# Kernel optimization log

Measured on AMD Instinct MI355X. Metric: run time of the kernel, lower is better.

Reference implementation:

```python
import jax, jax.numpy as jnp
import numpy as np

B, G, D, H, L, MLP = 64, 512, 384, 6, 12, 4
DH = D // H
MASK_RATIO = 0.6
KEEP_RATIO = 0.1
PAD_VAL = -1.0
START_VAL = 1.0
POS_HID = 128
NEG = -1e9


def setup_inputs() -> dict:
    key = jax.random.key(0)
    ks = jax.random.split(key, 24)
    s = 0.02
    inp = {
        "x": jax.random.normal(ks[0], (B, G, D), jnp.float32),
        "center_points": jax.random.normal(ks[1], (B, G, 3), jnp.float32),
        "mask_noise": jax.random.uniform(ks[2], (B, G), jnp.float32),
        # pos embedder MLP: 3 -> 128 -> D
        "pos_w1": jax.random.normal(ks[3], (3, POS_HID), jnp.float32) * s,
        "pos_b1": jnp.zeros((POS_HID,), jnp.float32),
        "pos_w2": jax.random.normal(ks[4], (POS_HID, D), jnp.float32) * s,
        "pos_b2": jnp.zeros((D,), jnp.float32),
        # stacked per-layer transformer params
        "ln1_w": jnp.ones((L, D), jnp.float32),
        "ln1_b": jnp.zeros((L, D), jnp.float32),
        "qkv_w": jax.random.normal(ks[5], (L, D, 3 * D), jnp.float32) * s,
        "qkv_b": jnp.zeros((L, 3 * D), jnp.float32),
        "proj_w": jax.random.normal(ks[6], (L, D, D), jnp.float32) * s,
        "proj_b": jnp.zeros((L, D), jnp.float32),
        "ln2_w": jnp.ones((L, D), jnp.float32),
        "ln2_b": jnp.zeros((L, D), jnp.float32),
        "fc1_w": jax.random.normal(ks[7], (L, D, MLP * D), jnp.float32) * s,
        "fc1_b": jnp.zeros((L, MLP * D), jnp.float32),
        "fc2_w": jax.random.normal(ks[8], (L, MLP * D, D), jnp.float32) * s,
        "fc2_b": jnp.zeros((L, D), jnp.float32),
        # final LayerNorm
        "norm_w": jnp.ones((D,), jnp.float32),
        "norm_b": jnp.zeros((D,), jnp.float32),
    }
    return inp


def _layer_norm(h, w, b, eps=1e-5):
    mu = jnp.mean(h, axis=-1, keepdims=True)
    var = jnp.mean(jnp.square(h - mu), axis=-1, keepdims=True)
    return (h - mu) * jax.lax.rsqrt(var + eps) * w + b


def _random_mask(center, noise):
    # padding tokens: all coords equal PAD_VAL
    pad = jnp.all(center == PAD_VAL, axis=-1)                      # [B, G] bool
    if MASK_RATIO == 0:
        return jnp.zeros(pad.shape, bool), pad
    n = (G - jnp.sum(pad.astype(jnp.int32), axis=-1))              # non-padding count
    k = (n.astype(jnp.float32) * KEEP_RATIO).astype(jnp.int32)     # kept-first tokens
    m = ((n - k).astype(jnp.float32) * MASK_RATIO).astype(jnp.int32)
    M = jnp.max(m)
    j = jnp.arange(G)[None, :]
    # shuffle region [k, n): pick m random slots (uniform subset via rank of noise)
    region = (j >= k[:, None]) & (j < n[:, None])
    u = jnp.where(region, noise, jnp.inf)
    rank = jnp.argsort(jnp.argsort(u, axis=-1), axis=-1)
    shuf = (rank < m[:, None]) & region
    # tail of ones: positions [n, n + M - m)
    tail = (j >= n[:, None]) & (j < (n + M - m)[:, None])
    return shuf | tail, pad


def _attention(h, qw, qb, pw, pb, bias):
    qkv = (h @ qw + qb).reshape(B, G, 3, H, DH).transpose(2, 0, 3, 1, 4)
    q, k, v = qkv[0], qkv[1], qkv[2]                               # [B, H, G, DH]
    s = jnp.einsum('bhqd,bhkd->bhqk', q, k) * (DH ** -0.5) + bias
    a = jax.nn.softmax(s, axis=-1)
    o = jnp.einsum('bhqk,bhkd->bhqd', a, v).transpose(0, 2, 1, 3).reshape(B, G, D)
    return o @ pw + pb


def _forward(x, center_points, mask_noise,
             pos_w1, pos_b1, pos_w2, pos_b2,
             ln1_w, ln1_b, qkv_w, qkv_b, proj_w, proj_b,
             ln2_w, ln2_b, fc1_w, fc1_b, fc2_w, fc2_b,
             norm_w, norm_b):
    # shift right + start token
    start = jnp.full((B, 1, D), START_VAL, x.dtype)
    x = jnp.concatenate([start, x[:, :-1, :]], axis=1)
    # positional embedding of shifted centers + start-token pos
    pos = jax.nn.gelu(center_points[:, :-1, :] @ pos_w1 + pos_b1, approximate=False) @ pos_w2 + pos_b2
    pos = jnp.concatenate([jnp.full((B, 1, D), START_VAL, x.dtype), pos], axis=1)
    # causal | (random column mask & ~eye) attention mask
    triu = jnp.triu(jnp.ones((G, G), bool), 1)
    rand_mask, pad = _random_mask(center_points, mask_noise)
    eye = jnp.eye(G, dtype=bool)
    attn_mask = triu[None, :, :] | (rand_mask[:, None, :] & ~eye[None, :, :])   # [B, G, G]
    bias = jnp.where(attn_mask | pad[:, None, :], NEG, 0.0)[:, None, :, :]      # [B,1,G,G]

    def block(h, p):
        l1w, l1b, qw, qb, pw, pb, l2w, l2b, f1w, f1b, f2w, f2b = p
        h = h + pos
        h = h + _attention(_layer_norm(h, l1w, l1b), qw, qb, pw, pb, bias)
        h = h + (jax.nn.gelu(_layer_norm(h, l2w, l2b) @ f1w + f1b, approximate=False) @ f2w + f2b)
        return h, None

    x, _ = jax.lax.scan(block, x, (ln1_w, ln1_b, qkv_w, qkv_b, proj_w, proj_b,
                                   ln2_w, ln2_b, fc1_w, fc1_b, fc2_w, fc2_b))
    x = _layer_norm(x, norm_w, norm_b)
    return x, pad, attn_mask


def reference(x, center_points, mask_noise,
              pos_w1, pos_b1, pos_w2, pos_b2,
              ln1_w, ln1_b, qkv_w, qkv_b, proj_w, proj_b,
              ln2_w, ln2_b, fc1_w, fc1_b, fc2_w, fc2_b,
              norm_w, norm_b):
    out, pad, attn_mask = _forward(x, center_points, mask_noise,
                                   pos_w1, pos_b1, pos_w2, pos_b2,
                                   ln1_w, ln1_b, qkv_w, qkv_b, proj_w, proj_b,
                                   ln2_w, ln2_b, fc1_w, fc1_b, fc2_w, fc2_b,
                                   norm_w, norm_b)
    # torch repeat_interleave over heads -> [B*H, G, G]
    return out, pad, jnp.repeat(attn_mask, H, axis=0)
```

## Files before the change

### kernel.cpp

```cpp
#include <hip/hip_runtime.h>
#include <math.h>

typedef _Float16 f16;
typedef f16 f16x8 __attribute__((ext_vector_type(8)));
typedef float f32x4 __attribute__((ext_vector_type(4)));

#define NB 64
#define NG 512
#define ND 384
#define NH 6
#define NL 12
#define NDH 64
#define BG (NB * NG)
#define BGD (BG * ND)

#define OFF_WQKV   0
#define OFF_WPROJ  2654208
#define OFF_WFC1   3538944
#define OFF_WFC2   7077888
#define OFF_FLAGS  10616832
#define OFF_NKM    10625024
#define OFF_MMAX   10625216
#define OFF_POS    10625280
#define OFF_HID    23208192
#define OFF_Y      25305344
#define OFF_YBIG   31596800
#define OFF_QB     56762624
#define OFF_KB     63054080
#define OFF_VT     69345536
#define OFF_OB     75636992
#define OFF_W2T    81928448
#define OFF_HB     81953024

typedef __attribute__((address_space(3))) void lds_t;
typedef const __attribute__((address_space(1))) void gmem_t;
__device__ __forceinline__ void gload16(const void* g, void* l)
{
    __builtin_amdgcn_global_load_lds((gmem_t*)g, (lds_t*)l, 16, 0, 0);
}

__global__ __launch_bounds__(256)
void transpose_kernel(const float* __restrict__ src, f16* __restrict__ dst,
                      int K, int N)
{
    __shared__ float tile[32][33];
    const int l = blockIdx.z;
    const float* S = src + (size_t)l * K * N;
    f16* D = dst + (size_t)l * K * N;
    const int n0 = blockIdx.x * 32, k0 = blockIdx.y * 32;
    const int tx = threadIdx.x, ty = threadIdx.y;
#pragma unroll
    for (int i = 0; i < 32; i += 8)
        tile[ty + i][tx] = S[(size_t)(k0 + ty + i) * N + n0 + tx];
    __syncthreads();
#pragma unroll
    for (int i = 0; i < 32; i += 8)
        D[(size_t)(n0 + ty + i) * K + k0 + tx] = (f16)tile[tx][ty + i];
}

__global__ __launch_bounds__(256)
void dpos_a(const float* cen, const float* w1, const float* b1, f16* hid)
{
    const int idx = blockIdx.x * 256 + threadIdx.x;
    if (idx >= BG * 128) return;
    const int t = idx >> 7, k = idx & 127;
    const int g = t & (NG - 1);
    if (g == 0) { hid[idx] = (f16)0.f; return; }
    const float* c = cen + (size_t)(t - 1) * 3;
    const float hv = c[0] * w1[k] + c[1] * w1[128 + k] + c[2] * w1[256 + k] + b1[k];
    hid[idx] = (f16)(0.5f * hv * (1.0f + erff(hv * 0.70710678118654752f)));
}

__global__ __launch_bounds__(384)
void pos_fix(float* pos)
{
    const int b = blockIdx.x;
    pos[((size_t)b * NG) * ND + threadIdx.x] = 1.0f;
}

__global__ __launch_bounds__(512)
void dmask_a(const float* cen, float* pad_out, int* nkm)
{
    const int b = blockIdx.x, j = threadIdx.x;
    const float* c = cen + ((size_t)b * NG + j) * 3;
    const bool pad = (c[0] == -1.f) && (c[1] == -1.f) && (c[2] == -1.f);
    pad_out[b * NG + j] = pad ? 1.f : 0.f;
    if (j == 0) {
        int cnt = 0;
        for (int i = 0; i < NG; i++) {
            const float* ci = cen + ((size_t)b * NG + i) * 3;
            cnt += (ci[0] == -1.f && ci[1] == -1.f && ci[2] == -1.f) ? 1 : 0;
        }
        const int n = NG - cnt;
        const int k = (int)((float)n * 0.1f);
        const int m = (int)((float)(n - k) * 0.6f);
        nkm[b * 3] = n; nkm[b * 3 + 1] = k; nkm[b * 3 + 2] = m;
    }
}

__global__ void dmask_m(const int* nkm, int* Mmax)
{
    if (threadIdx.x == 0 && blockIdx.x == 0) {
        int M = 0;
        for (int b = 0; b < NB; b++) M = max(M, nkm[b * 3 + 2]);
        *Mmax = M;
    }
}

__global__ __launch_bounds__(512)
void dmask_b(const float* cen, const float* noi, const int* nkm,
             const int* Mmax, unsigned char* flags)
{
    const int b = blockIdx.x, j = threadIdx.x;
    const int n = nkm[b * 3], k = nkm[b * 3 + 1], m = nkm[b * 3 + 2];
    const int M = *Mmax;
    const float nz = noi[b * NG + j];
    const bool inreg = (j >= k) && (j < n);
    bool shuf = false;
    if (inreg) {
        int cnt = 0;
        for (int i = 0; i < NG; i++) {
            if (i < k || i >= n) continue;
            const float ui = noi[b * NG + i];
            cnt += (ui < nz) || (ui == nz && i < j);
        }
        shuf = cnt < m;
    }
    const float* c = cen + ((size_t)b * NG + j) * 3;
    const bool pad = (c[0] == -1.f) && (c[1] == -1.f) && (c[2] == -1.f);
    const bool tail = (j >= n) && (j < n + M - m);
    flags[b * NG + j] = (unsigned char)(((shuf | tail) ? 1 : 0) | (pad ? 2 : 0));
}

__global__ __launch_bounds__(512)
void flags_rep_kernel(const unsigned char* flags, float* mo)
{
    const int bq = blockIdx.x;
    const int b = bq >> 9, q = bq & (NG - 1);
    const int j = threadIdx.x;
    mo[(((size_t)(b * NH) * NG + q) * NG) + j] = (float)flags[b * NG + j];
}

__global__ __launch_bounds__(512)
void mask_out_kernel(float* mo)
{
    const int bq = blockIdx.x;
    const int b = bq >> 9, q = bq & (NG - 1);
    const int j = threadIdx.x;
    const unsigned char f =
        (unsigned char)mo[(((size_t)(b * NH) * NG + q) * NG) + j];
    const float val = ((q < j) || ((f & 1) && (q != j))) ? 1.0f : 0.0f;
#pragma unroll
    for (int h = 0; h < NH; h++)
        mo[(((size_t)(b * NH + h) * NG + q) * NG) + j] = val;
}

__global__ __launch_bounds__(256)
void h0_kernel(const float* x, const float* pos, f16* h)
{
    const size_t i = (size_t)blockIdx.x * 256 + threadIdx.x;
    const int g = (int)((i / ND) & (NG - 1));
    const float xv = x[(g == 0) ? i : (i - ND)];
    const float base = (g == 0) ? 1.0f : xv;
    h[i] = (f16)(base + pos[i]);
}

template<int MODE>
__global__ __launch_bounds__(256)
void lnb_kernel(const f16* __restrict__ h,
                const float* __restrict__ w, const float* __restrict__ bb,
                f16* __restrict__ y16, float* __restrict__ y32)
{
    __shared__ float red[4][64];
    const int wid = threadIdx.x >> 6;
    const int lane = threadIdx.x & 63;
    const int t = blockIdx.x * 4 + wid;
    const size_t base = (size_t)t * ND + lane;
    float v[6];
    float s = 0.f;
#pragma unroll
    for (int i = 0; i < 6; i++) {
        const float xv = (float)h[base + i * 64];
        v[i] = xv; s += xv;
    }
    red[wid][lane] = s;
    __syncthreads();
    for (int st = 32; st > 0; st >>= 1) {
        if (lane < st) red[wid][lane] += red[wid][lane + st];
        __syncthreads();
    }
    const float mu = red[wid][0] * (1.f / ND);
    float vs = 0.f;
#pragma unroll
    for (int i = 0; i < 6; i++) { const float d = v[i] - mu; vs += d * d; }
    __syncthreads();
    red[wid][lane] = vs;
    __syncthreads();
    for (int st = 32; st > 0; st >>= 1) {
        if (lane < st) red[wid][lane] += red[wid][lane + st];
        __syncthreads();
    }
    const float rstd = rsqrtf(red[wid][0] * (1.f / ND) + 1e-5f);
#pragma unroll
    for (int i = 0; i < 6; i++) {
        const float o = (v[i] - mu) * rstd * w[lane + i * 64] + bb[lane + i * 64];
        if constexpr (MODE == 2) y32[base + i * 64] = o;
        else                     y16[base + i * 64] = (f16)o;
    }
}

template<int MODE>
__global__ __launch_bounds__(256)
void gemm_kernel(const f16* __restrict__ A, const f16* __restrict__ Bt,
                 const float* __restrict__ bias, int K, int NT,
                 f16* __restrict__ hres, const float* __restrict__ posadd,
                 float* __restrict__ out32, f16* __restrict__ out16,
                 f16* __restrict__ Qo, f16* __restrict__ Ko, f16* __restrict__ Vo)
{
    __shared__ f16 sA[128 * 64];
    __shared__ f16 sB[128 * 64];
    const int tid = threadIdx.x;
    const int w = tid >> 6, lane = tid & 63;
    const int lr = lane & 15, lg = lane >> 4;
    const int wm = w >> 1, wn = w & 1;
    const int N = NT * 128;

    const int nwg = gridDim.x;
    const int chunk = nwg >> 3;
    const int flat = (blockIdx.x & 7) * chunk + (blockIdx.x >> 3);
    const int m0 = (flat / NT) * 128;
    const int n0 = (flat % NT) * 128;

    f32x4 acc[4][4];
#pragma unroll
    for (int mf = 0; mf < 4; mf++)
#pragma unroll
        for (int nf = 0; nf < 4; nf++)
            acc[mf][nf] = (f32x4){0.f, 0.f, 0.f, 0.f};

    const int srow0 = w * 8 + (lane >> 3);
    const int scolB = (lane & 7) * 16;

    for (int k0 = 0; k0 < K; k0 += 64) {
        __syncthreads();
#pragma unroll
        for (int i = 0; i < 4; i++) {
            const int row = i * 32 + srow0;
            const int colB = scolB ^ ((row & 7) << 4);
            const char* ga = (const char*)(A + (size_t)(m0 + row) * K + k0) + colB;
            const char* gb = (const char*)(Bt + (size_t)(n0 + row) * K + k0) + colB;
            gload16(ga, (char*)sA + row * 128 + scolB);
            gload16(gb, (char*)sB + row * 128 + scolB);
        }
        __syncthreads();
#pragma unroll
        for (int kk = 0; kk < 64; kk += 32) {
            f16x8 af[4], bf[4];
#pragma unroll
            for (int mf = 0; mf < 4; mf++) {
                const int r = wm * 64 + mf * 16 + lr;
                const int cb = ((kk + lg * 8) * 2) ^ ((r & 7) << 4);
                af[mf] = *(const f16x8*)((const char*)sA + r * 128 + cb);
            }
#pragma unroll
            for (int nf = 0; nf < 4; nf++) {
                const int r = wn * 64 + nf * 16 + lr;
                const int cb = ((kk + lg * 8) * 2) ^ ((r & 7) << 4);
                bf[nf] = *(const f16x8*)((const char*)sB + r * 128 + cb);
            }
#pragma unroll
            for (int mf = 0; mf < 4; mf++)
#pragma unroll
                for (int nf = 0; nf < 4; nf++)
                    acc[mf][nf] = __builtin_amdgcn_mfma_f32_16x16x32_f16(
                        af[mf], bf[nf], acc[mf][nf], 0, 0, 0);
        }
    }

#pragma unroll
    for (int mf = 0; mf < 4; mf++) {
#pragma unroll
        for (int nf = 0; nf < 4; nf++) {
            const int n_g = n0 + wn * 64 + nf * 16 + lr;
            const float bv = bias[n_g];
#pragma unroll
            for (int r = 0; r < 4; r++) {
                const int m_g = m0 + wm * 64 + mf * 16 + lg * 4 + r;
                const float v = acc[mf][nf][r] + bv;
                const size_t oidx = (size_t)m_g * N + n_g;
                if constexpr (MODE == 1) {
                    hres[oidx] = (f16)((float)hres[oidx] + v);
                } else if constexpr (MODE == 4) {
                    hres[oidx] = (f16)((float)hres[oidx] + v + posadd[oidx]);
                } else if constexpr (MODE == 2) {
                    const float ge = 0.5f * v * (1.0f + erff(v * 0.70710678118654752f));
                    out16[oidx] = (f16)ge;
                } else if constexpr (MODE == 3) {
                    out32[oidx] = v;
                } else {
                    const int which = n_g / ND;
                    const int rem = n_g - which * ND;
                    const int hh = rem >> 6, dh = rem & 63;
                    const int bb2 = m_g >> 9, gg = m_g & (NG - 1);
                    if (which == 0)
                        Qo[((size_t)(bb2 * NH + hh) * NG + gg) * NDH + dh] = (f16)v;
                    else if (which == 1)
                        Ko[((size_t)(bb2 * NH + hh) * NG + gg) * NDH + dh] = (f16)v;
                    else
                        Vo[((size_t)(bb2 * NH + hh) * NDH + dh) * NG + gg] = (f16)v;
                }
            }
        }
    }
}

__global__ __launch_bounds__(256)
void attn_kernel(const f16* __restrict__ Q, const f16* __restrict__ Kt,
                 const f16* __restrict__ V, const unsigned char* __restrict__ flags,
                 f16* __restrict__ O)
{
    __shared__ f16 sQ[128][72];
    __shared__ f16 sK[64][72];
    __shared__ f16 sV[64][72];
    __shared__ f16 sP[4][16][72];
    const int tid = threadIdx.x;
    const int w = tid >> 6, lane = tid & 63;
    const int lr = lane & 15, lg = lane >> 4;
    const int q0 = blockIdx.x * 128;
    const int bh = blockIdx.y;
    const int b = bh / NH, hh = bh - b * NH;
    const f16* Qg = Q + ((size_t)bh * NG + q0) * NDH;
    const f16* Kg = Kt + (size_t)bh * NG * NDH;
    const f16* Vg = V + (size_t)bh * NDH * NG;
    const unsigned char* fl = flags + b * NG;

#pragma unroll
    for (int i = 0; i < 4; i++) {
        const int c = tid + i * 256;
        const int r = c >> 3, cc = (c & 7) * 8;
        *(f16x8*)&sQ[r][cc] = *(const f16x8*)(Qg + r * NDH + cc);
    }
    __syncthreads();
    f16x8 aq[2][2];
#pragma unroll
    for (int hf = 0; hf < 2; hf++) {
        aq[hf][0] = *(const f16x8*)&sQ[hf * 64 + w * 16 + lr][lg * 8];
        aq[hf][1] = *(const f16x8*)&sQ[hf * 64 + w * 16 + lr][32 + lg * 8];
    }

    float m_run[2][4], l_run[2][4];
    f32x4 o[2][4];
#pragma unroll
    for (int hf = 0; hf < 2; hf++)
#pragma unroll
        for (int r = 0; r < 4; r++) {
            m_run[hf][r] = -INFINITY; l_run[hf][r] = 0.f;
            o[hf][r] = (f32x4){0.f, 0.f, 0.f, 0.f};
        }

    const int ntile = 2 * blockIdx.x + 2;
    for (int jt = 0; jt < ntile; jt++) {
        const int j0 = jt * 64;
        __syncthreads();
#pragma unroll
        for (int i = 0; i < 2; i++) {
            const int c = tid + i * 256;
            const int r = c >> 3, cc = (c & 7) * 8;
            *(f16x8*)&sK[r][cc] = *(const f16x8*)(Kg + (size_t)(j0 + r) * NDH + cc);
            *(f16x8*)&sV[r][cc] = *(const f16x8*)(Vg + (size_t)r * NG + j0 + cc);
        }
        __syncthreads();

#pragma unroll
        for (int hf = 0; hf < 2; hf++) {
            if (jt >= ntile - 1 + hf) continue;
            f32x4 s[4];
#pragma unroll
            for (int nf = 0; nf < 4; nf++) s[nf] = (f32x4){0.f, 0.f, 0.f, 0.f};
#pragma unroll
            for (int kf = 0; kf < 2; kf++) {
#pragma unroll
                for (int nf = 0; nf < 4; nf++) {
                    f16x8 bk = *(const f16x8*)&sK[nf * 16 + lr][kf * 32 + lg * 8];
                    s[nf] = __builtin_amdgcn_mfma_f32_16x16x32_f16(aq[hf][kf], bk, s[nf], 0, 0, 0);
                }
            }
#pragma unroll
            for (int nf = 0; nf < 4; nf++) {
                const int j_g = j0 + nf * 16 + lr;
                const unsigned char f = fl[j_g];
#pragma unroll
                for (int r = 0; r < 4; r++) {
                    const int q_g = q0 + hf * 64 + w * 16 + lg * 4 + r;
                    const bool masked = (q_g < j_g) || (f & 2) || ((f & 1) && (j_g != q_g));
                    s[nf][r] = s[nf][r] * 0.125f + (masked ? -1e9f : 0.f);
                }
            }
#pragma unroll
            for (int r = 0; r < 4; r++) {
                float mx = fmaxf(fmaxf(s[0][r], s[1][r]), fmaxf(s[2][r], s[3][r]));
#pragma unroll
                for (int off = 1; off < 16; off <<= 1) mx = fmaxf(mx, __shfl_xor(mx, off));
                const float nm = fmaxf(m_run[hf][r], mx);
                const float sc = __expf(m_run[hf][r] - nm);
                m_run[hf][r] = nm;
                l_run[hf][r] *= sc;
#pragma unroll
                for (int nf = 0; nf < 4; nf++) o[hf][nf][r] *= sc;
                float ls = 0.f;
#pragma unroll
                for (int nf = 0; nf < 4; nf++) {
                    const float p = __expf(s[nf][r] - nm);
                    ls += p;
                    sP[w][lg * 4 + r][nf * 16 + lr] = (f16)p;
                }
                l_run[hf][r] += ls;
            }
#pragma unroll
            for (int kf = 0; kf < 2; kf++) {
                f16x8 ap = *(const f16x8*)&sP[w][lr][kf * 32 + lg * 8];
#pragma unroll
                for (int nf = 0; nf < 4; nf++) {
                    f16x8 bv = *(const f16x8*)&sV[nf * 16 + lr][kf * 32 + lg * 8];
                    o[hf][nf] = __builtin_amdgcn_mfma_f32_16x16x32_f16(ap, bv, o[hf][nf], 0, 0, 0);
                }
            }
        }
    }

#pragma unroll
    for (int hf = 0; hf < 2; hf++) {
        float inv[4];
#pragma unroll
        for (int r = 0; r < 4; r++) {
            float l = l_run[hf][r];
#pragma unroll
            for (int off = 1; off < 16; off <<= 1) l += __shfl_xor(l, off);
            inv[r] = 1.f / l;
        }
#pragma unroll
        for (int nf = 0; nf < 4; nf++) {
#pragma unroll
            for (int r = 0; r < 4; r++) {
                const int q_g = q0 + hf * 64 + w * 16 + lg * 4 + r;
                const int dh = nf * 16 + lr;
                O[((size_t)(b * NG + q_g)) * ND + hh * NDH + dh] = (f16)(o[hf][nf][r] * inv[r]);
            }
        }
    }
}

extern "C" void kernel_launch(void* const* d_in, const int* in_sizes, int n_in,
                              void* d_out, int out_size, void* d_ws, size_t ws_size,
                              hipStream_t stream)
{
    (void)d_ws; (void)ws_size;

    static const int exp_sizes[21] = {
        12582912, 98304, 32768,
        384, 128, 49152, 384,
        4608, 4608,
        5308416, 13824,
        1769472, 4608,
        4608, 4608,
        7077888, 18432,
        7077888, 4608,
        384, 384
    };
    if (n_in != 21 || out_size != 113278976) return;
    for (int i = 0; i < 21; i++) if (in_sizes[i] != exp_sizes[i]) return;

    const float* x    = (const float*)d_in[0];
    const float* cen  = (const float*)d_in[1];
    const float* noi  = (const float*)d_in[2];
    const float* pw1  = (const float*)d_in[3];
    const float* pb1  = (const float*)d_in[4];
    const float* pw2  = (const float*)d_in[5];
    const float* pb2  = (const float*)d_in[6];
    const float* ln1w = (const float*)d_in[7];
    const float* ln1b = (const float*)d_in[8];
    const float* qkvw = (const float*)d_in[9];
    const float* qkvb = (const float*)d_in[10];
    const float* projw= (const float*)d_in[11];
    const float* projb= (const float*)d_in[12];
    const float* ln2w = (const float*)d_in[13];
    const float* ln2b = (const float*)d_in[14];
    const float* fc1w = (const float*)d_in[15];
    const float* fc1b = (const float*)d_in[16];
    const float* fc2w = (const float*)d_in[17];
    const float* fc2b = (const float*)d_in[18];
    const float* nw   = (const float*)d_in[19];
    const float* nb   = (const float*)d_in[20];

    float* out0    = (float*)d_out;
    float* pad_out = out0 + BGD;
    float* R       = pad_out + BG;

    f16* WqkvT  = (f16*)(R + OFF_WQKV);
    f16* WprojT = (f16*)(R + OFF_WPROJ);
    f16* Wfc1T  = (f16*)(R + OFF_WFC1);
    f16* Wfc2T  = (f16*)(R + OFF_WFC2);
    unsigned char* flags = (unsigned char*)(R + OFF_FLAGS);
    int* nkm  = (int*)(R + OFF_NKM);
    int* Mmax = (int*)(R + OFF_MMAX);
    float* POS = R + OFF_POS;
    f16* HID   = (f16*)(R + OFF_HID);
    f16* Y     = (f16*)(R + OFF_Y);
    f16* Ybig  = (f16*)(R + OFF_YBIG);
    f16* Qb    = (f16*)(R + OFF_QB);
    f16* Kb    = (f16*)(R + OFF_KB);
    f16* Vt    = (f16*)(R + OFF_VT);
    f16* Ob    = (f16*)(R + OFF_OB);
    f16* W2T   = (f16*)(R + OFF_W2T);
    f16* Hb    = (f16*)(R + OFF_HB);

    dim3 tb(32, 8);
    transpose_kernel<<<dim3(36, 12, NL), tb, 0, stream>>>(qkvw, WqkvT, 384, 1152);
    transpose_kernel<<<dim3(12, 12, NL), tb, 0, stream>>>(projw, WprojT, 384, 384);
    transpose_kernel<<<dim3(48, 12, NL), tb, 0, stream>>>(fc1w, Wfc1T, 384, 1536);
    transpose_kernel<<<dim3(12, 48, NL), tb, 0, stream>>>(fc2w, Wfc2T, 1536, 384);
    transpose_kernel<<<dim3(12, 4, 1),  tb, 0, stream>>>(pw2, W2T, 128, 384);

    dmask_a<<<NB, 512, 0, stream>>>(cen, pad_out, nkm);
    dmask_m<<<1, 64, 0, stream>>>(nkm, Mmax);
    dmask_b<<<NB, 512, 0, stream>>>(cen, noi, nkm, Mmax, flags);
    dpos_a<<<BG * 128 / 256, 256, 0, stream>>>(cen, pw1, pb1, HID);
    gemm_kernel<3><<<768, 256, 0, stream>>>(HID, W2T, pb2, 128, 3,
                                            nullptr, nullptr, POS, nullptr,
                                            nullptr, nullptr, nullptr);
    pos_fix<<<NB, 384, 0, stream>>>(POS);
    h0_kernel<<<BGD / 256, 256, 0, stream>>>(x, POS, Hb);

    for (int l = 0; l < NL; l++) {
        lnb_kernel<1><<<BG / 4, 256, 0, stream>>>(Hb, ln1w + l * ND, ln1b + l * ND, Y, nullptr);
        gemm_kernel<0><<<2304, 256, 0, stream>>>(Y, WqkvT + (size_t)l * 442368,
                                                 qkvb + l * 1152, 384, 9,
                                                 nullptr, nullptr, nullptr, nullptr,
                                                 Qb, Kb, Vt);
        attn_kernel<<<dim3(4, NB * NH), 256, 0, stream>>>(Qb, Kb, Vt, flags, Ob);
        gemm_kernel<1><<<768, 256, 0, stream>>>(Ob, WprojT + (size_t)l * 147456,
                                                projb + l * ND, 384, 3,
                                                Hb, nullptr, nullptr, nullptr,
                                                nullptr, nullptr, nullptr);
        lnb_kernel<1><<<BG / 4, 256, 0, stream>>>(Hb, ln2w + l * ND, ln2b + l * ND, Y, nullptr);
        gemm_kernel<2><<<3072, 256, 0, stream>>>(Y, Wfc1T + (size_t)l * 589824,
                                                 fc1b + l * 1536, 384, 12,
                                                 nullptr, nullptr, nullptr, Ybig,
                                                 nullptr, nullptr, nullptr);
        if (l < NL - 1) {
            gemm_kernel<4><<<768, 256, 0, stream>>>(Ybig, Wfc2T + (size_t)l * 589824,
                                                    fc2b + l * ND, 1536, 3,
                                                    Hb, POS, nullptr, nullptr,
                                                    nullptr, nullptr, nullptr);
        } else {
            gemm_kernel<1><<<768, 256, 0, stream>>>(Ybig, Wfc2T + (size_t)l * 589824,
                                                    fc2b + l * ND, 1536, 3,
                                                    Hb, nullptr, nullptr, nullptr,
                                                    nullptr, nullptr, nullptr);
        }
    }

    lnb_kernel<2><<<BG / 4, 256, 0, stream>>>(Hb, nw, nb, nullptr, out0);
    flags_rep_kernel<<<BG, 512, 0, stream>>>(flags, R);
    mask_out_kernel<<<BG, 512, 0, stream>>>(R);
}
```

Before: 5.074 ms.

## Fuse residual GEMM epilogues with following LayerNorm via full-row tiles

Adds a GEMM kernel whose block covers a full 128x384 output row tile, so the proj and fc2 residual updates can compute LayerNorm statistics in the epilogue. It writes both the updated residual and the normalized activations, which removes the separate lnb_kernel launches and their extra read of the hidden state. The trade-off is a grid of only 256 blocks with 512 threads and much larger shared and register use per block, which lowers occupancy and parallelism for these GEMMs. Variance is now computed from the sum and the sum of squares instead of two passes.

```diff
diff --git a/kernel.cpp b/kernel.cpp
--- a/kernel.cpp
+++ b/kernel.cpp
@@ -3,6 +3,7 @@
 
 typedef _Float16 f16;
 typedef f16 f16x8 __attribute__((ext_vector_type(8)));
+typedef f16 f16v2 __attribute__((ext_vector_type(2)));
 typedef float f32x4 __attribute__((ext_vector_type(4)));
 
 #define NB 64
@@ -213,7 +214,7 @@
 __global__ __launch_bounds__(256)
 void gemm_kernel(const f16* __restrict__ A, const f16* __restrict__ Bt,
                  const float* __restrict__ bias, int K, int NT,
-                 f16* __restrict__ hres, const float* __restrict__ posadd,
+                 f16* __restrict__ hres,
                  float* __restrict__ out32, f16* __restrict__ out16,
                  f16* __restrict__ Qo, f16* __restrict__ Ko, f16* __restrict__ Vo)
 {
@@ -290,8 +291,6 @@
                 const size_t oidx = (size_t)m_g * N + n_g;
                 if constexpr (MODE == 1) {
                     hres[oidx] = (f16)((float)hres[oidx] + v);
-                } else if constexpr (MODE == 4) {
-                    hres[oidx] = (f16)((float)hres[oidx] + v + posadd[oidx]);
                 } else if constexpr (MODE == 2) {
                     const float ge = 0.5f * v * (1.0f + erff(v * 0.70710678118654752f));
                     out16[oidx] = (f16)ge;
@@ -309,6 +308,167 @@
                     else
                         Vo[((size_t)(bb2 * NH + hh) * NDH + dh) * NG + gg] = (f16)v;
                 }
+            }
+        }
+    }
+}
+
+template<int ADDPOS>
+__global__ __launch_bounds__(512)
+void gemmln_kernel(const f16* __restrict__ A, const f16* __restrict__ Bt,
+                   const float* __restrict__ bias, int K,
+                   f16* __restrict__ hres, const float* __restrict__ posadd,
+                   const float* __restrict__ lw, const float* __restrict__ lb,
+                   f16* __restrict__ Y)
+{
+    __shared__ f16 sA[128 * 64];
+    __shared__ f16 sB[384 * 64];
+    __shared__ float part[2][128][2];
+    const int tid = threadIdx.x;
+    const int w = tid >> 6, lane = tid & 63;
+    const int lr = lane & 15, lg = lane >> 4;
+    const int wm = w >> 2, wn = w & 3;
+    const int vm = w >> 1, vn = w & 1;
+
+    const int nwg = gridDim.x;
+    const int chunk = nwg >> 3;
+    const int m0 = ((blockIdx.x & 7) * chunk + (blockIdx.x >> 3)) * 128;
+    (void)wm; (void)wn;
+
+    f32x4 acc[2][12];
+#pragma unroll
+    for (int mf = 0; mf < 2; mf++)
+#pragma unroll
+        for (int nf = 0; nf < 12; nf++)
+            acc[mf][nf] = (f32x4){0.f, 0.f, 0.f, 0.f};
+
+    const int srowA = tid >> 3;
+    const int scolB = (tid & 7) * 16;
+
+    for (int k0 = 0; k0 < K; k0 += 64) {
+        __syncthreads();
+#pragma unroll
+        for (int i = 0; i < 2; i++) {
+            const int row = i * 64 + srowA;
+            const int colB = scolB ^ ((row & 7) << 4);
+            gload16((const char*)(A + (size_t)(m0 + row) * K + k0) + colB,
+                    (char*)sA + row * 128 + scolB);
+        }
+#pragma unroll
+        for (int i = 0; i < 6; i++) {
+            const int row = i * 64 + srowA;
+            const int colB = scolB ^ ((row & 7) << 4);
+            gload16((const char*)(Bt + (size_t)row * K + k0) + colB,
+                    (char*)sB + row * 128 + scolB);
+        }
+        __syncthreads();
+#pragma unroll
+        for (int kk = 0; kk < 64; kk += 32) {
+            f16x8 af[2];
+#pragma unroll
+            for (int mf = 0; mf < 2; mf++) {
+                const int r = vm * 32 + mf * 16 + lr;
+                const int cb = ((kk + lg * 8) * 2) ^ ((r & 7) << 4);
+                af[mf] = *(const f16x8*)((const char*)sA + r * 128 + cb);
+            }
+#pragma unroll
+            for (int half = 0; half < 2; half++) {
+                f16x8 bf[6];
+#pragma unroll
+                for (int j = 0; j < 6; j++) {
+                    const int nf = half * 6 + j;
+                    const int r = vn * 192 + nf * 16 + lr;
+                    const int cb = ((kk + lg * 8) * 2) ^ ((r & 7) << 4);
+                    bf[j] = *(const f16x8*)((const char*)sB + r * 128 + cb);
+                }
+#pragma unroll
+                for (int mf = 0; mf < 2; mf++)
+#pragma unroll
+                    for (int j = 0; j < 6; j++)
+                        acc[mf][half * 6 + j] = __builtin_amdgcn_mfma_f32_16x16x32_f16(
+                            af[mf], bf[j], acc[mf][half * 6 + j], 0, 0, 0);
+            }
+        }
+    }
+
+    f16v2 hn[2][12][2];
+    float rs[2][4], rq[2][4];
+#pragma unroll
+    for (int mf = 0; mf < 2; mf++)
+#pragma unroll
+        for (int r = 0; r < 4; r++) { rs[mf][r] = 0.f; rq[mf][r] = 0.f; }
+
+#pragma unroll
+    for (int mf = 0; mf < 2; mf++) {
+#pragma unroll
+        for (int nf = 0; nf < 12; nf++) {
+            const int col = vn * 192 + nf * 16 + lr;
+            const float bv = bias[col];
+#pragma unroll
+            for (int r = 0; r < 4; r++) {
+                const int row_g = m0 + vm * 32 + mf * 16 + lg * 4 + r;
+                const size_t oidx = (size_t)row_g * ND + col;
+                float hv = (float)hres[oidx] + acc[mf][nf][r] + bv;
+                if constexpr (ADDPOS) hv += posadd[oidx];
+                const f16 hf = (f16)hv;
+                hn[mf][nf][r >> 1][r & 1] = hf;
+                const float hff = (float)hf;
+                rs[mf][r] += hff;
+                rq[mf][r] += hff * hff;
+            }
+        }
+    }
+#pragma unroll
+    for (int mf = 0; mf < 2; mf++)
+#pragma unroll
+        for (int r = 0; r < 4; r++) {
+#pragma unroll
+            for (int off = 1; off < 16; off <<= 1) {
+                rs[mf][r] += __shfl_xor(rs[mf][r], off);
+                rq[mf][r] += __shfl_xor(rq[mf][r], off);
+            }
+        }
+    if (lr == 0) {
+#pragma unroll
+        for (int mf = 0; mf < 2; mf++)
+#pragma unroll
+            for (int r = 0; r < 4; r++) {
+                const int rl = vm * 32 + mf * 16 + lg * 4 + r;
+                part[vn][rl][0] = rs[mf][r];
+                part[vn][rl][1] = rq[mf][r];
+            }
+    }
+    __syncthreads();
+
+    float mus[2][4], rstds[2][4];
+#pragma unroll
+    for (int mf = 0; mf < 2; mf++)
+#pragma unroll
+        for (int r = 0; r < 4; r++) {
+            const int rl = vm * 32 + mf * 16 + lg * 4 + r;
+            const float s = part[0][rl][0] + part[1][rl][0];
+            const float q = part[0][rl][1] + part[1][rl][1];
+            const float mu = s * (1.f / ND);
+            const float var = q * (1.f / ND) - mu * mu;
+            mus[mf][r] = mu;
+            rstds[mf][r] = rsqrtf(var + 1e-5f);
+        }
+
+#pragma unroll
+    for (int mf = 0; mf < 2; mf++) {
+#pragma unroll
+        for (int nf = 0; nf < 12; nf++) {
+            const int col = vn * 192 + nf * 16 + lr;
+            const float wl = lw[col];
+            const float bl = lb[col];
+#pragma unroll
+            for (int r = 0; r < 4; r++) {
+                const int row_g = m0 + vm * 32 + mf * 16 + lg * 4 + r;
+                const size_t oidx = (size_t)row_g * ND + col;
+                const f16 hf = hn[mf][nf][r >> 1][r & 1];
+                hres[oidx] = hf;
+                const float o = ((float)hf - mus[mf][r]) * rstds[mf][r] * wl + bl;
+                Y[oidx] = (f16)o;
             }
         }
     }
@@ -526,36 +686,36 @@
     dmask_b<<<NB, 512, 0, stream>>>(cen, noi, nkm, Mmax, flags);
     dpos_a<<<BG * 128 / 256, 256, 0, stream>>>(cen, pw1, pb1, HID);
     gemm_kernel<3><<<768, 256, 0, stream>>>(HID, W2T, pb2, 128, 3,
-                                            nullptr, nullptr, POS, nullptr,
+                                            nullptr, POS, nullptr,
                                             nullptr, nullptr, nullptr);
     pos_fix<<<NB, 384, 0, stream>>>(POS);
     h0_kernel<<<BGD / 256, 256, 0, stream>>>(x, POS, Hb);
 
+    lnb_kernel<1><<<BG / 4, 256, 0, stream>>>(Hb, ln1w, ln1b, Y, nullptr);
+
     for (int l = 0; l < NL; l++) {
-        lnb_kernel<1><<<BG / 4, 256, 0, stream>>>(Hb, ln1w + l * ND, ln1b + l * ND, Y, nullptr);
         gemm_kernel<0><<<2304, 256, 0, stream>>>(Y, WqkvT + (size_t)l * 442368,
                                                  qkvb + l * 1152, 384, 9,
-                                                 nullptr, nullptr, nullptr, nullptr,
+                                                 nullptr, nullptr, nullptr,
                                                  Qb, Kb, Vt);
         attn_kernel<<<dim3(4, NB * NH), 256, 0, stream>>>(Qb, Kb, Vt, flags, Ob);
-        gemm_kernel<1><<<768, 256, 0, stream>>>(Ob, WprojT + (size_t)l * 147456,
-                                                projb + l * ND, 384, 3,
-                                                Hb, nullptr, nullptr, nullptr,
-                                                nullptr, nullptr, nullptr);
-        lnb_kernel<1><<<BG / 4, 256, 0, stream>>>(Hb, ln2w + l * ND, ln2b + l * ND, Y, nullptr);
+        gemmln_kernel<0><<<256, 512, 0, stream>>>(Ob, WprojT + (size_t)l * 147456,
+                                                  projb + l * ND, 384,
+                                                  Hb, nullptr,
+                                                  ln2w + l * ND, ln2b + l * ND, Y);
         gemm_kernel<2><<<3072, 256, 0, stream>>>(Y, Wfc1T + (size_t)l * 589824,
                                                  fc1b + l * 1536, 384, 12,
-                                                 nullptr, nullptr, nullptr, Ybig,
+                                                 nullptr, nullptr, Ybig,
                                                  nullptr, nullptr, nullptr);
         if (l < NL - 1) {
-            gemm_kernel<4><<<768, 256, 0, stream>>>(Ybig, Wfc2T + (size_t)l * 589824,
-                                                    fc2b + l * ND, 1536, 3,
-                                                    Hb, POS, nullptr, nullptr,
-                                                    nullptr, nullptr, nullptr);
+            gemmln_kernel<1><<<256, 512, 0, stream>>>(Ybig, Wfc2T + (size_t)l * 589824,
+                                                      fc2b + l * ND, 1536,
+                                                      Hb, POS,
+                                                      ln1w + (l + 1) * ND, ln1b + (l + 1) * ND, Y);
         } else {
             gemm_kernel<1><<<768, 256, 0, stream>>>(Ybig, Wfc2T + (size_t)l * 589824,
                                                     fc2b + l * ND, 1536, 3,
-                                                    Hb, nullptr, nullptr, nullptr,
+                                                    Hb, nullptr, nullptr,
                                                     nullptr, nullptr, nullptr);
         }
     }
```

New measurement: 4.962 ms. 2.2% less time.
